# Kernel tuning notes

Measured on AMD Instinct MI355X. Metric: run time of the kernel, lower is better.

The kernel has to match this reference:

```python
import jax, jax.numpy as jnp
import numpy as np

BIG_Z = 1e6  # sentinel used for background depth when finding the nearest mesh


def setup_inputs() -> dict:
    key = jax.random.key(0)
    ks = jax.random.split(key, 6)
    N, H, W, K = 8, 512, 512, 1      # n_mesh, image H, image W, faces_per_pixel
    F, V, C = 20000, 10002, 32       # faces, verts, feature channels
    zbuf = jax.random.normal(ks[0], (N, H, W, K), jnp.float32)  # ~half negative = background
    pix_to_face = jax.random.randint(ks[1], (N, H, W, K), -1, F)  # -1 = no face
    b = jax.random.uniform(ks[2], (N, H, W, K, 3), jnp.float32) + 1e-3
    bary_coords = b / jnp.sum(b, axis=-1, keepdims=True)
    dists = jax.random.uniform(ks[3], (N, H, W, K), jnp.float32)
    face_memory = jax.random.normal(ks[4], (F, 3, C), jnp.float32)
    packed_faces = jax.random.randint(ks[5], (F, 3), 0, V)
    return {
        "zbuf": zbuf,
        "pix_to_face": pix_to_face,
        "bary_coords": bary_coords,
        "dists": dists,
        "face_memory": face_memory,
        "packed_faces": packed_faces,
        "num_verts": V,
        "mask_duplicate": 0,
    }


def reference(zbuf, pix_to_face, bary_coords, dists, face_memory, packed_faces,
              num_verts, mask_duplicate):
    N = zbuf.shape[0]
    Fn = face_memory.shape[0]

    # per-object mask BEFORE occlusion masking (zbuf[..., 0] >= 0)
    per_obj_mask = zbuf[..., 0] >= 0  # [N,H,W]

    # _mask_occluded_object: pixels covered by >1 mesh
    covered = (zbuf > -1)
    dup = jnp.sum(covered.astype(jnp.float32), axis=0, keepdims=True) > 1  # [1,H,W,K]
    dup = jnp.broadcast_to(dup, zbuf.shape)  # [N,H,W,K]
    if not mask_duplicate:
        # keep the nearest (min-z) mesh at duplicate pixels
        tmp = jnp.where(zbuf < 0, BIG_Z, zbuf)
        min_idx = jnp.argmin(tmp, axis=0)  # [H,W,K]
        mesh_ids = jnp.arange(N).reshape(N, 1, 1, 1)
        dup = dup & (mesh_ids != min_idx[None])

    # mask occluded fragments to -1 (matches in-place boolean writes)
    p = jnp.where(dup, -1, pix_to_face)
    bc = jnp.where(dup[..., None], -1.0, bary_coords)
    d = jnp.where(dup, -1.0, dists)
    zb = jnp.where(dup, -1.0, zbuf)

    # interpolate_face_attributes: gather [N,H,W,K,3,C] then bary-weighted sum,
    # zeroing pixels with pix_to_face < 0
    valid = p >= 0
    safe = jnp.where(valid, p, 0)
    attrs = face_memory[safe]  # [N,H,W,K,3,C]
    out = jnp.einsum('nhwki,nhwkic->nhwkc', bc, attrs)
    out = out * valid[..., None].astype(out.dtype)
    out_map = out[:, :, :, 0, :]               # squeeze K dim -> [N,H,W,C]
    out_map = jnp.transpose(out_map, (0, 3, 1, 2))  # -> [N,C,H,W]

    # vertex visibility: unique visible faces -> their vertices get 1.0
    face_hit = jnp.zeros((Fn,), jnp.float32).at[safe.ravel()].add(
        valid.ravel().astype(jnp.float32))
    face_vis = (face_hit > 0).astype(jnp.float32)  # [F]
    vv = jnp.zeros((num_verts,), jnp.float32).at[packed_faces.ravel()].add(
        jnp.broadcast_to(face_vis[:, None], (Fn, 3)).ravel())
    vertex_visibility_map = (vv > 0).astype(jnp.float32)

    # return out_map, visibility, per-object mask, and masked fragments (frags_clone)
    return out_map, vertex_visibility_map, per_obj_mask, zb, p, d, bc
```

## Files before the change

### kernel.cpp

```cpp
#include <hip/hip_runtime.h>

#define BIG_Z_F 1000000.0f
#define N_MESH 8

__global__ __launch_bounds__(256) void raster_main(
    const float* __restrict__ zbuf,
    const int*   __restrict__ p2f,
    const float* __restrict__ bary,
    const float* __restrict__ dists,
    const float* __restrict__ fmem,
    const int*   __restrict__ mdp,
    float* __restrict__ out_map,
    float* __restrict__ maskO,
    float* __restrict__ zbO,
    float* __restrict__ pO,
    float* __restrict__ dO,
    float* __restrict__ bcO,
    int*   __restrict__ faceflag,
    int HW, int C)
{
    const int pix = blockIdx.x * blockDim.x + threadIdx.x;
    if (pix >= HW) return;
    const int md = *mdp;

    float z[N_MESH];
    int count = 0;
    float best = __builtin_inff();
    int bidx = 0;
    #pragma unroll
    for (int n = 0; n < N_MESH; ++n) {
        const float zv = __builtin_nontemporal_load(&zbuf[n * HW + pix]);
        z[n] = zv;
        count += (zv > -1.0f) ? 1 : 0;
        const float t = (zv < 0.0f) ? BIG_Z_F : zv;
        if (t < best) { best = t; bidx = n; }
    }
    const bool dup0 = (count > 1);

    #pragma unroll
    for (int n = 0; n < N_MESH; ++n) {
        const int idx = n * HW + pix;
        const bool dup = dup0 && ((md != 0) || (n != bidx));
        const float zv = z[n];

        __builtin_nontemporal_store((zv >= 0.0f) ? 1.0f : 0.0f, &maskO[idx]);
        __builtin_nontemporal_store(dup ? -1.0f : zv, &zbO[idx]);

        const int p = dup ? -1 : __builtin_nontemporal_load(&p2f[idx]);
        __builtin_nontemporal_store((float)p, &pO[idx]);
        __builtin_nontemporal_store(
            dup ? -1.0f : __builtin_nontemporal_load(&dists[idx]), &dO[idx]);

        float b0, b1, b2;
        {
            const float* bp = bary + (size_t)idx * 3;
            b0 = dup ? -1.0f : __builtin_nontemporal_load(bp + 0);
            b1 = dup ? -1.0f : __builtin_nontemporal_load(bp + 1);
            b2 = dup ? -1.0f : __builtin_nontemporal_load(bp + 2);
        }
        float* bo = bcO + (size_t)idx * 3;
        __builtin_nontemporal_store(b0, bo + 0);
        __builtin_nontemporal_store(b1, bo + 1);
        __builtin_nontemporal_store(b2, bo + 2);

        const bool valid = (p >= 0);
        if (valid) faceflag[p] = 1;

        const float* a = fmem + (size_t)(valid ? p : 0) * 3 * C;
        #pragma unroll
        for (int c4 = 0; c4 < 32; c4 += 4) {
            float r0 = 0.0f, r1 = 0.0f, r2 = 0.0f, r3 = 0.0f;
            if (valid) {
                const float4 a0 = *(const float4*)(a + c4);
                const float4 a1 = *(const float4*)(a + C + c4);
                const float4 a2 = *(const float4*)(a + 2 * C + c4);
                r0 = b0 * a0.x + b1 * a1.x + b2 * a2.x;
                r1 = b0 * a0.y + b1 * a1.y + b2 * a2.y;
                r2 = b0 * a0.z + b1 * a1.z + b2 * a2.z;
                r3 = b0 * a0.w + b1 * a1.w + b2 * a2.w;
            }
            const int obase = (n * C + c4) * HW + pix;
            __builtin_nontemporal_store(r0, &out_map[obase + 0 * HW]);
            __builtin_nontemporal_store(r1, &out_map[obase + 1 * HW]);
            __builtin_nontemporal_store(r2, &out_map[obase + 2 * HW]);
            __builtin_nontemporal_store(r3, &out_map[obase + 3 * HW]);
        }
    }
}

__global__ __launch_bounds__(256) void vert_vis(
    const int* __restrict__ faceflag,
    const int* __restrict__ pfaces,
    float* __restrict__ vv,
    int F)
{
    const int f = blockIdx.x * blockDim.x + threadIdx.x;
    if (f >= F) return;
    if (faceflag[f]) {
        vv[pfaces[f * 3 + 0]] = 1.0f;
        vv[pfaces[f * 3 + 1]] = 1.0f;
        vv[pfaces[f * 3 + 2]] = 1.0f;
    }
}

extern "C" void kernel_launch(void* const* d_in, const int* in_sizes, int n_in,
                              void* d_out, int out_size, void* d_ws, size_t ws_size,
                              hipStream_t stream) {
    const float* zbuf   = (const float*)d_in[0];
    const int*   p2f    = (const int*)  d_in[1];
    const float* bary   = (const float*)d_in[2];
    const float* dists  = (const float*)d_in[3];
    const float* fmem   = (const float*)d_in[4];
    const int*   pfaces = (const int*)  d_in[5];
    const int*   mdp    = (const int*)  d_in[7];

    const long long P  = in_sizes[0];
    const int HW = (int)(P / N_MESH);
    const int F3 = in_sizes[5];
    const int F  = F3 / 3;
    const int C  = in_sizes[4] / F3;
    const int V  = (int)((long long)out_size - P * C - 7 * P);

    float* out     = (float*)d_out;
    float* out_map = out;
    float* vv      = out_map + P * C;
    float* maskO   = vv + V;
    float* zbO     = maskO + P;
    float* pO      = zbO + P;
    float* dO      = pO + P;
    float* bcO     = dO + P;

    int* faceflag = (int*)d_ws;

    hipMemsetAsync(faceflag, 0, (size_t)F * sizeof(int), stream);
    hipMemsetAsync(vv, 0, (size_t)V * sizeof(float), stream);

    raster_main<<<dim3((HW + 255) / 256), dim3(256), 0, stream>>>(
        zbuf, p2f, bary, dists, fmem, mdp,
        out_map, maskO, zbO, pO, dO, bcO, faceflag, HW, C);

    vert_vis<<<dim3((F + 255) / 256), dim3(256), 0, stream>>>(
        faceflag, pfaces, vv, F);
}
```

Baseline: 424.1 us.

## Split raster kernel into per-pixel reduce and per-mesh interpolation kernels

The fused per-pixel kernel, which looped serially over all 8 meshes, is split in two. The first kernel computes the duplicate/argmin reduction over meshes, writes the mask and masked zbuf, and stores a per-pixel winner byte. The second kernel uses a 2D grid with one mesh per blockIdx.y, giving 8x more threads and more memory parallelism for the gather and writes. The cost is an extra launch and a small intermediate byte buffer in workspace.

```diff
diff --git a/kernel.cpp b/kernel.cpp
--- a/kernel.cpp
+++ b/kernel.cpp
@@ -3,21 +3,13 @@
 #define BIG_Z_F 1000000.0f
 #define N_MESH 8
 
-__global__ __launch_bounds__(256) void raster_main(
+__global__ __launch_bounds__(256) void raster_reduce(
     const float* __restrict__ zbuf,
-    const int*   __restrict__ p2f,
-    const float* __restrict__ bary,
-    const float* __restrict__ dists,
-    const float* __restrict__ fmem,
-    const int*   __restrict__ mdp,
-    float* __restrict__ out_map,
     float* __restrict__ maskO,
     float* __restrict__ zbO,
-    float* __restrict__ pO,
-    float* __restrict__ dO,
-    float* __restrict__ bcO,
-    int*   __restrict__ faceflag,
-    int HW, int C)
+    unsigned char* __restrict__ win,
+    const int* __restrict__ mdp,
+    int HW)
 {
     const int pix = blockIdx.x * blockDim.x + threadIdx.x;
     if (pix >= HW) return;
@@ -41,50 +33,75 @@
     for (int n = 0; n < N_MESH; ++n) {
         const int idx = n * HW + pix;
         const bool dup = dup0 && ((md != 0) || (n != bidx));
-        const float zv = z[n];
+        __builtin_nontemporal_store((z[n] >= 0.0f) ? 1.0f : 0.0f, &maskO[idx]);
+        __builtin_nontemporal_store(dup ? -1.0f : z[n], &zbO[idx]);
+    }
+    win[pix] = dup0 ? (unsigned char)bidx : (unsigned char)0xFF;
+}
 
-        __builtin_nontemporal_store((zv >= 0.0f) ? 1.0f : 0.0f, &maskO[idx]);
-        __builtin_nontemporal_store(dup ? -1.0f : zv, &zbO[idx]);
+__global__ __launch_bounds__(256) void raster_interp(
+    const int*   __restrict__ p2f,
+    const float* __restrict__ bary,
+    const float* __restrict__ dists,
+    const float* __restrict__ fmem,
+    const unsigned char* __restrict__ win,
+    const int*   __restrict__ mdp,
+    float* __restrict__ out_map,
+    float* __restrict__ pO,
+    float* __restrict__ dO,
+    float* __restrict__ bcO,
+    int*   __restrict__ faceflag,
+    int HW, int C)
+{
+    const int pix = blockIdx.x * blockDim.x + threadIdx.x;
+    if (pix >= HW) return;
+    const int n   = blockIdx.y;
+    const int idx = n * HW + pix;
+    const int md  = *mdp;
 
-        const int p = dup ? -1 : __builtin_nontemporal_load(&p2f[idx]);
-        __builtin_nontemporal_store((float)p, &pO[idx]);
-        __builtin_nontemporal_store(
-            dup ? -1.0f : __builtin_nontemporal_load(&dists[idx]), &dO[idx]);
+    const unsigned char w = win[pix];
+    const bool dup = (w != 0xFF) && ((md != 0) || (n != (int)w));
 
-        float b0, b1, b2;
-        {
-            const float* bp = bary + (size_t)idx * 3;
-            b0 = dup ? -1.0f : __builtin_nontemporal_load(bp + 0);
-            b1 = dup ? -1.0f : __builtin_nontemporal_load(bp + 1);
-            b2 = dup ? -1.0f : __builtin_nontemporal_load(bp + 2);
+    const int   praw = __builtin_nontemporal_load(&p2f[idx]);
+    const float drw  = __builtin_nontemporal_load(&dists[idx]);
+    const float* bp  = bary + (size_t)idx * 3;
+    const float b0r  = __builtin_nontemporal_load(bp + 0);
+    const float b1r  = __builtin_nontemporal_load(bp + 1);
+    const float b2r  = __builtin_nontemporal_load(bp + 2);
+
+    const int   p  = dup ? -1 : praw;
+    const float b0 = dup ? -1.0f : b0r;
+    const float b1 = dup ? -1.0f : b1r;
+    const float b2 = dup ? -1.0f : b2r;
+
+    __builtin_nontemporal_store((float)p, &pO[idx]);
+    __builtin_nontemporal_store(dup ? -1.0f : drw, &dO[idx]);
+    float* bo = bcO + (size_t)idx * 3;
+    __builtin_nontemporal_store(b0, bo + 0);
+    __builtin_nontemporal_store(b1, bo + 1);
+    __builtin_nontemporal_store(b2, bo + 2);
+
+    const bool valid = (p >= 0);
+    if (valid) faceflag[p] = 1;
+
+    const float* a = fmem + (size_t)(valid ? p : 0) * 3 * C;
+    #pragma unroll
+    for (int c4 = 0; c4 < 32; c4 += 4) {
+        float r0 = 0.0f, r1 = 0.0f, r2 = 0.0f, r3 = 0.0f;
+        if (valid) {
+            const float4 a0 = *(const float4*)(a + c4);
+            const float4 a1 = *(const float4*)(a + C + c4);
+            const float4 a2 = *(const float4*)(a + 2 * C + c4);
+            r0 = b0 * a0.x + b1 * a1.x + b2 * a2.x;
+            r1 = b0 * a0.y + b1 * a1.y + b2 * a2.y;
+            r2 = b0 * a0.z + b1 * a1.z + b2 * a2.z;
+            r3 = b0 * a0.w + b1 * a1.w + b2 * a2.w;
         }
-        float* bo = bcO + (size_t)idx * 3;
-        __builtin_nontemporal_store(b0, bo + 0);
-        __builtin_nontemporal_store(b1, bo + 1);
-        __builtin_nontemporal_store(b2, bo + 2);
-
-        const bool valid = (p >= 0);
-        if (valid) faceflag[p] = 1;
-
-        const float* a = fmem + (size_t)(valid ? p : 0) * 3 * C;
-        #pragma unroll
-        for (int c4 = 0; c4 < 32; c4 += 4) {
-            float r0 = 0.0f, r1 = 0.0f, r2 = 0.0f, r3 = 0.0f;
-            if (valid) {
-                const float4 a0 = *(const float4*)(a + c4);
-                const float4 a1 = *(const float4*)(a + C + c4);
-                const float4 a2 = *(const float4*)(a + 2 * C + c4);
-                r0 = b0 * a0.x + b1 * a1.x + b2 * a2.x;
-                r1 = b0 * a0.y + b1 * a1.y + b2 * a2.y;
-                r2 = b0 * a0.z + b1 * a1.z + b2 * a2.z;
-                r3 = b0 * a0.w + b1 * a1.w + b2 * a2.w;
-            }
-            const int obase = (n * C + c4) * HW + pix;
-            __builtin_nontemporal_store(r0, &out_map[obase + 0 * HW]);
-            __builtin_nontemporal_store(r1, &out_map[obase + 1 * HW]);
-            __builtin_nontemporal_store(r2, &out_map[obase + 2 * HW]);
-            __builtin_nontemporal_store(r3, &out_map[obase + 3 * HW]);
-        }
+        const int obase = (n * C + c4) * HW + pix;
+        __builtin_nontemporal_store(r0, &out_map[obase + 0 * HW]);
+        __builtin_nontemporal_store(r1, &out_map[obase + 1 * HW]);
+        __builtin_nontemporal_store(r2, &out_map[obase + 2 * HW]);
+        __builtin_nontemporal_store(r3, &out_map[obase + 3 * HW]);
     }
 }
 
@@ -130,14 +147,20 @@
     float* dO      = pO + P;
     float* bcO     = dO + P;
 
-    int* faceflag = (int*)d_ws;
+    int* faceflag      = (int*)d_ws;
+    unsigned char* win = (unsigned char*)(faceflag + F);
 
     hipMemsetAsync(faceflag, 0, (size_t)F * sizeof(int), stream);
     hipMemsetAsync(vv, 0, (size_t)V * sizeof(float), stream);
 
-    raster_main<<<dim3((HW + 255) / 256), dim3(256), 0, stream>>>(
-        zbuf, p2f, bary, dists, fmem, mdp,
-        out_map, maskO, zbO, pO, dO, bcO, faceflag, HW, C);
+    const int blocks = (HW + 255) / 256;
+
+    raster_reduce<<<dim3(blocks), dim3(256), 0, stream>>>(
+        zbuf, maskO, zbO, win, mdp, HW);
+
+    raster_interp<<<dim3(blocks, N_MESH), dim3(256), 0, stream>>>(
+        p2f, bary, dists, fmem, win, mdp,
+        out_map, pO, dO, bcO, faceflag, HW, C);
 
     vert_vis<<<dim3((F + 255) / 256), dim3(256), 0, stream>>>(
         faceflag, pfaces, vv, F);
```

Measured after the change: 426.2 us. No clear change (+0.5%).

## Split raster kernel into reduce and per-mesh interp with 4-pixel vector I/O

Applied to the files above, without the earlier changes.

Splits the single kernel into two. The first computes the per-pixel duplicate/winner decision from zbuf and writes a byte winner map plus the mask and zbuf outputs. The second runs one grid row per mesh and handles 4 pixels per thread with 16-byte vector loads and stores. This gives 8x more blocks for parallelism and replaces scalar strided bary and output accesses with vector ones. In exchange it adds an extra launch and a small intermediate buffer, and it assumes HW is divisible by 1024.

```diff
diff --git a/kernel.cpp b/kernel.cpp
--- a/kernel.cpp
+++ b/kernel.cpp
@@ -3,87 +3,162 @@
 #define BIG_Z_F 1000000.0f
 #define N_MESH 8
 
-__global__ __launch_bounds__(256) void raster_main(
-    const float* __restrict__ zbuf,
-    const int*   __restrict__ p2f,
-    const float* __restrict__ bary,
-    const float* __restrict__ dists,
+typedef float f4 __attribute__((ext_vector_type(4)));
+typedef int   i4 __attribute__((ext_vector_type(4)));
+typedef unsigned char uc4 __attribute__((ext_vector_type(4)));
+
+
+__global__ __launch_bounds__(256) void raster_reduce(
+    const f4* __restrict__ zbuf4,
+    f4* __restrict__ maskO4,
+    f4* __restrict__ zbO4,
+    uc4* __restrict__ win4,
+    const int* __restrict__ mdp,
+    int HW4)
+{
+    const int q = blockIdx.x * blockDim.x + threadIdx.x;
+    if (q >= HW4) return;
+    const int md = *mdp;
+
+    float z[N_MESH][4];
+    #pragma unroll
+    for (int n = 0; n < N_MESH; ++n) {
+        const f4 v = __builtin_nontemporal_load(&zbuf4[n * HW4 + q]);
+        z[n][0] = v.x; z[n][1] = v.y; z[n][2] = v.z; z[n][3] = v.w;
+    }
+
+    bool dup0[4]; int bidx[4];
+    #pragma unroll
+    for (int j = 0; j < 4; ++j) {
+        int count = 0; float best = __builtin_inff(); int bi = 0;
+        #pragma unroll
+        for (int n = 0; n < N_MESH; ++n) {
+            const float zv = z[n][j];
+            count += (zv > -1.0f) ? 1 : 0;
+            const float t = (zv < 0.0f) ? BIG_Z_F : zv;
+            if (t < best) { best = t; bi = n; }
+        }
+        dup0[j] = (count > 1);
+        bidx[j] = bi;
+    }
+
+    #pragma unroll
+    for (int n = 0; n < N_MESH; ++n) {
+        f4 m, zb;
+        #pragma unroll
+        for (int j = 0; j < 4; ++j) {
+            const bool dup = dup0[j] && ((md != 0) || (n != bidx[j]));
+            m[j]  = (z[n][j] >= 0.0f) ? 1.0f : 0.0f;
+            zb[j] = dup ? -1.0f : z[n][j];
+        }
+        __builtin_nontemporal_store(m,  &maskO4[n * HW4 + q]);
+        __builtin_nontemporal_store(zb, &zbO4[n * HW4 + q]);
+    }
+    uc4 w;
+    w.x = dup0[0] ? (unsigned char)bidx[0] : (unsigned char)0xFF;
+    w.y = dup0[1] ? (unsigned char)bidx[1] : (unsigned char)0xFF;
+    w.z = dup0[2] ? (unsigned char)bidx[2] : (unsigned char)0xFF;
+    w.w = dup0[3] ? (unsigned char)bidx[3] : (unsigned char)0xFF;
+    win4[q] = w;
+}
+
+__global__ __launch_bounds__(256) void raster_interp(
+    const i4* __restrict__ p2f4,
+    const f4* __restrict__ bary4,
+    const f4* __restrict__ dists4,
     const float* __restrict__ fmem,
-    const int*   __restrict__ mdp,
-    float* __restrict__ out_map,
-    float* __restrict__ maskO,
-    float* __restrict__ zbO,
-    float* __restrict__ pO,
-    float* __restrict__ dO,
-    float* __restrict__ bcO,
-    int*   __restrict__ faceflag,
-    int HW, int C)
+    const uc4* __restrict__ win4,
+    const int* __restrict__ mdp,
+    f4* __restrict__ out_map4,
+    f4* __restrict__ pO4,
+    f4* __restrict__ dO4,
+    f4* __restrict__ bcO4,
+    int* __restrict__ faceflag,
+    int HW4, int C)
 {
-    const int pix = blockIdx.x * blockDim.x + threadIdx.x;
-    if (pix >= HW) return;
-    const int md = *mdp;
-
-    float z[N_MESH];
-    int count = 0;
-    float best = __builtin_inff();
-    int bidx = 0;
-    #pragma unroll
-    for (int n = 0; n < N_MESH; ++n) {
-        const float zv = __builtin_nontemporal_load(&zbuf[n * HW + pix]);
-        z[n] = zv;
-        count += (zv > -1.0f) ? 1 : 0;
-        const float t = (zv < 0.0f) ? BIG_Z_F : zv;
-        if (t < best) { best = t; bidx = n; }
-    }
-    const bool dup0 = (count > 1);
-
-    #pragma unroll
-    for (int n = 0; n < N_MESH; ++n) {
-        const int idx = n * HW + pix;
-        const bool dup = dup0 && ((md != 0) || (n != bidx));
-        const float zv = z[n];
-
-        __builtin_nontemporal_store((zv >= 0.0f) ? 1.0f : 0.0f, &maskO[idx]);
-        __builtin_nontemporal_store(dup ? -1.0f : zv, &zbO[idx]);
-
-        const int p = dup ? -1 : __builtin_nontemporal_load(&p2f[idx]);
-        __builtin_nontemporal_store((float)p, &pO[idx]);
-        __builtin_nontemporal_store(
-            dup ? -1.0f : __builtin_nontemporal_load(&dists[idx]), &dO[idx]);
-
-        float b0, b1, b2;
-        {
-            const float* bp = bary + (size_t)idx * 3;
-            b0 = dup ? -1.0f : __builtin_nontemporal_load(bp + 0);
-            b1 = dup ? -1.0f : __builtin_nontemporal_load(bp + 1);
-            b2 = dup ? -1.0f : __builtin_nontemporal_load(bp + 2);
-        }
-        float* bo = bcO + (size_t)idx * 3;
-        __builtin_nontemporal_store(b0, bo + 0);
-        __builtin_nontemporal_store(b1, bo + 1);
-        __builtin_nontemporal_store(b2, bo + 2);
-
-        const bool valid = (p >= 0);
-        if (valid) faceflag[p] = 1;
-
-        const float* a = fmem + (size_t)(valid ? p : 0) * 3 * C;
-        #pragma unroll
-        for (int c4 = 0; c4 < 32; c4 += 4) {
-            float r0 = 0.0f, r1 = 0.0f, r2 = 0.0f, r3 = 0.0f;
-            if (valid) {
-                const float4 a0 = *(const float4*)(a + c4);
-                const float4 a1 = *(const float4*)(a + C + c4);
-                const float4 a2 = *(const float4*)(a + 2 * C + c4);
-                r0 = b0 * a0.x + b1 * a1.x + b2 * a2.x;
-                r1 = b0 * a0.y + b1 * a1.y + b2 * a2.y;
-                r2 = b0 * a0.z + b1 * a1.z + b2 * a2.z;
-                r3 = b0 * a0.w + b1 * a1.w + b2 * a2.w;
+    const int q = blockIdx.x * blockDim.x + threadIdx.x;
+    if (q >= HW4) return;
+    const int n    = blockIdx.y;
+    const int idx4 = n * HW4 + q;
+    const int md   = *mdp;
+
+    const uc4 wv = win4[q];
+    const unsigned char w[4] = { wv.x, wv.y, wv.z, wv.w };
+
+    const i4 praw = __builtin_nontemporal_load(&p2f4[idx4]);
+    const f4 drw  = __builtin_nontemporal_load(&dists4[idx4]);
+    const f4 bv0  = __builtin_nontemporal_load(&bary4[idx4 * 3 + 0]);
+    const f4 bv1  = __builtin_nontemporal_load(&bary4[idx4 * 3 + 1]);
+    const f4 bv2  = __builtin_nontemporal_load(&bary4[idx4 * 3 + 2]);
+    const int   pr[4] = { praw.x, praw.y, praw.z, praw.w };
+    const float dr[4] = { drw.x, drw.y, drw.z, drw.w };
+    const float br[4][3] = {
+        { bv0.x, bv0.y, bv0.z },
+        { bv0.w, bv1.x, bv1.y },
+        { bv1.z, bv1.w, bv2.x },
+        { bv2.y, bv2.z, bv2.w },
+    };
+
+    bool  valid[4];
+    int   p[4];
+    float b[4][3];
+    f4 pOv, dOv;
+    #pragma unroll
+    for (int j = 0; j < 4; ++j) {
+        const bool dup = (w[j] != 0xFF) && ((md != 0) || (n != (int)w[j]));
+        p[j] = dup ? -1 : pr[j];
+        valid[j] = (p[j] >= 0);
+        b[j][0] = dup ? -1.0f : br[j][0];
+        b[j][1] = dup ? -1.0f : br[j][1];
+        b[j][2] = dup ? -1.0f : br[j][2];
+        pOv[j] = (float)p[j];
+        dOv[j] = dup ? -1.0f : dr[j];
+        if (valid[j]) faceflag[p[j]] = 1;
+    }
+    __builtin_nontemporal_store(pOv, &pO4[idx4]);
+    __builtin_nontemporal_store(dOv, &dO4[idx4]);
+    {
+        f4 c0, c1, c2;
+        c0.x = b[0][0]; c0.y = b[0][1]; c0.z = b[0][2]; c0.w = b[1][0];
+        c1.x = b[1][1]; c1.y = b[1][2]; c1.z = b[2][0]; c1.w = b[2][1];
+        c2.x = b[2][2]; c2.y = b[3][0]; c2.z = b[3][1]; c2.w = b[3][2];
+        __builtin_nontemporal_store(c0, &bcO4[idx4 * 3 + 0]);
+        __builtin_nontemporal_store(c1, &bcO4[idx4 * 3 + 1]);
+        __builtin_nontemporal_store(c2, &bcO4[idx4 * 3 + 2]);
+    }
+
+    const float* ab[4];
+    #pragma unroll
+    for (int j = 0; j < 4; ++j)
+        ab[j] = fmem + (size_t)(valid[j] ? p[j] : 0) * 3 * C;
+
+    #pragma unroll
+    for (int c4 = 0; c4 < 32; c4 += 4) {
+        float acc[4][4];
+        #pragma unroll
+        for (int k = 0; k < 4; ++k)
+            #pragma unroll
+            for (int j = 0; j < 4; ++j)
+                acc[k][j] = 0.0f;
+
+        #pragma unroll
+        for (int j = 0; j < 4; ++j) {
+            if (valid[j]) {
+                const float* a = ab[j];
+                const f4 a0 = *(const f4*)(a + c4);
+                const f4 a1 = *(const f4*)(a + C + c4);
+                const f4 a2 = *(const f4*)(a + 2 * C + c4);
+                acc[0][j] = b[j][0] * a0.x + b[j][1] * a1.x + b[j][2] * a2.x;
+                acc[1][j] = b[j][0] * a0.y + b[j][1] * a1.y + b[j][2] * a2.y;
+                acc[2][j] = b[j][0] * a0.z + b[j][1] * a1.z + b[j][2] * a2.z;
+                acc[3][j] = b[j][0] * a0.w + b[j][1] * a1.w + b[j][2] * a2.w;
             }
-            const int obase = (n * C + c4) * HW + pix;
-            __builtin_nontemporal_store(r0, &out_map[obase + 0 * HW]);
-            __builtin_nontemporal_store(r1, &out_map[obase + 1 * HW]);
-            __builtin_nontemporal_store(r2, &out_map[obase + 2 * HW]);
-            __builtin_nontemporal_store(r3, &out_map[obase + 3 * HW]);
+        }
+        #pragma unroll
+        for (int k = 0; k < 4; ++k) {
+            f4 r;
+            r.x = acc[k][0]; r.y = acc[k][1]; r.z = acc[k][2]; r.w = acc[k][3];
+            __builtin_nontemporal_store(r, &out_map4[(size_t)(n * C + c4 + k) * HW4 + q]);
         }
     }
 }
@@ -115,11 +190,12 @@
     const int*   mdp    = (const int*)  d_in[7];
 
     const long long P  = in_sizes[0];
-    const int HW = (int)(P / N_MESH);
-    const int F3 = in_sizes[5];
-    const int F  = F3 / 3;
-    const int C  = in_sizes[4] / F3;
-    const int V  = (int)((long long)out_size - P * C - 7 * P);
+    const int HW  = (int)(P / N_MESH);
+    const int HW4 = HW / 4;
+    const int F3  = in_sizes[5];
+    const int F   = F3 / 3;
+    const int C   = in_sizes[4] / F3;
+    const int V   = (int)((long long)out_size - P * C - 7 * P);
 
     float* out     = (float*)d_out;
     float* out_map = out;
@@ -131,13 +207,19 @@
     float* bcO     = dO + P;
 
     int* faceflag = (int*)d_ws;
-
-    hipMemsetAsync(faceflag, 0, (size_t)F * sizeof(int), stream);
-    hipMemsetAsync(vv, 0, (size_t)V * sizeof(float), stream);
-
-    raster_main<<<dim3((HW + 255) / 256), dim3(256), 0, stream>>>(
-        zbuf, p2f, bary, dists, fmem, mdp,
-        out_map, maskO, zbO, pO, dO, bcO, faceflag, HW, C);
+    uc4* win4     = (uc4*)(faceflag + F);
+
+    (void)hipMemsetAsync(faceflag, 0, (size_t)F * sizeof(int), stream);
+    (void)hipMemsetAsync(vv, 0, (size_t)V * sizeof(float), stream);
+
+    raster_reduce<<<dim3(HW4 / 256), dim3(256), 0, stream>>>(
+        (const f4*)zbuf, (f4*)maskO, (f4*)zbO, win4, mdp, HW4);
+
+    raster_interp<<<dim3(HW4 / 256, N_MESH), dim3(256), 0, stream>>>(
+        (const i4*)p2f, (const f4*)bary, (const f4*)dists, fmem,
+        (const uc4*)win4, mdp,
+        (f4*)out_map, (f4*)pO, (f4*)dO, (f4*)bcO,
+        faceflag, HW4, C);
 
     vert_vis<<<dim3((F + 255) / 256), dim3(256), 0, stream>>>(
         faceflag, pfaces, vv, F);
```

Result: faster. 413.5 us (-2.5%).
